# Kernel optimization log

Measured on AMD Instinct MI355X. Metric: run time of the kernel, lower is better.

Reference implementation:

```python
import jax, jax.numpy as jnp
import numpy as np

N_PATCHES = 14
HIDDEN_D = 768
N_HEADS = 12
D_HEAD = HIDDEN_D // N_HEADS
SEQ = N_PATCHES ** 2 + 1  # 197
INPUT_D = 3 * 16 * 16  # c * patch_h * patch_w = 768
LN_EPS = 1e-5


def positional_embeddings(seq_len, d):
    # result[i, j] = sin(i / 10000**(j/d)) if j even else cos(i / 10000**((j-1)/d))
    i = jnp.arange(seq_len, dtype=jnp.float32)[:, None]
    j = jnp.arange(d, dtype=jnp.float32)[None, :]
    even = (jnp.arange(d) % 2 == 0)[None, :]
    denom_even = jnp.power(10000.0, j / d)
    denom_odd = jnp.power(10000.0, (j - 1.0) / d)
    return jnp.where(even, jnp.sin(i / denom_even), jnp.cos(i / denom_odd))


def setup_inputs() -> dict:
    key = jax.random.key(0)
    ks = jax.random.split(key, 12)
    s = 0.02
    return {
        "images": jax.random.normal(ks[0], (128, 3, 224, 224), dtype=jnp.float32),
        "W_map": jax.random.normal(ks[1], (HIDDEN_D, INPUT_D), dtype=jnp.float32) * s,
        "b_map": jax.random.normal(ks[2], (HIDDEN_D,), dtype=jnp.float32) * s,
        "class_token": jax.random.uniform(ks[3], (1, HIDDEN_D), dtype=jnp.float32),
        "ln_w": jnp.ones((SEQ, HIDDEN_D), dtype=jnp.float32),
        "ln_b": jnp.zeros((SEQ, HIDDEN_D), dtype=jnp.float32),
        "Wq": jax.random.normal(ks[4], (N_HEADS, D_HEAD, D_HEAD), dtype=jnp.float32) * s,
        "bq": jax.random.normal(ks[5], (N_HEADS, D_HEAD), dtype=jnp.float32) * s,
        "Wk": jax.random.normal(ks[6], (N_HEADS, D_HEAD, D_HEAD), dtype=jnp.float32) * s,
        "bk": jax.random.normal(ks[7], (N_HEADS, D_HEAD), dtype=jnp.float32) * s,
        "Wv": jax.random.normal(ks[8], (N_HEADS, D_HEAD, D_HEAD), dtype=jnp.float32) * s,
        "bv": jax.random.normal(ks[9], (N_HEADS, D_HEAD), dtype=jnp.float32) * s,
    }


def _forward(images, W_map, b_map, class_token, ln_w, ln_b, Wq, bq, Wk, bk, Wv, bv):
    n = images.shape[0]
    # naive patchify (faithful to source: a plain reshape)
    patches = images.reshape(n, N_PATCHES ** 2, INPUT_D)
    # linear mapper: x @ W.T + b
    tokens = jnp.einsum("npi,di->npd", patches, W_map) + b_map
    # prepend class token
    cls = jnp.broadcast_to(class_token[None], (n, 1, HIDDEN_D))
    tokens = jnp.concatenate([cls, tokens], axis=1)  # [n, SEQ, D]
    # positional embeddings
    tokens = tokens + positional_embeddings(SEQ, HIDDEN_D)[None]
    # LayerNorm over last two dims (SEQ, D) jointly
    mean = jnp.mean(tokens, axis=(-2, -1), keepdims=True)
    var = jnp.var(tokens, axis=(-2, -1), keepdims=True)
    x = (tokens - mean) / jnp.sqrt(var + LN_EPS) * ln_w + ln_b
    # multi-head self-attention (batched over samples and heads)
    xh = x.reshape(n, SEQ, N_HEADS, D_HEAD)  # head-sliced channels
    q = jnp.einsum("bshd,hed->bshe", xh, Wq) + bq[None, None]
    k = jnp.einsum("bshd,hed->bshe", xh, Wk) + bk[None, None]
    v = jnp.einsum("bshd,hed->bshe", xh, Wv) + bv[None, None]
    att = jax.nn.softmax(
        jnp.einsum("bshd,bthd->bhst", q, k) / jnp.sqrt(jnp.float32(D_HEAD)), axis=-1
    )
    msa = jnp.einsum("bhst,bthd->bshd", att, v).reshape(n, SEQ, HIDDEN_D)
    return tokens + msa


def reference(images, W_map, b_map, class_token, ln_w, ln_b, Wq, bq, Wk, bk, Wv, bv):
    return _forward(images, W_map, b_map, class_token, ln_w, ln_b, Wq, bq, Wk, bk, Wv, bv)
```

## Files before the change

kernel.cpp:

```cpp
#include <hip/hip_runtime.h>

typedef float fx4 __attribute__((ext_vector_type(4)));
typedef __bf16 bf16x8 __attribute__((ext_vector_type(8)));
typedef unsigned short ushort8 __attribute__((ext_vector_type(8)));
typedef unsigned int uint2v __attribute__((ext_vector_type(2)));
typedef unsigned int uint4v __attribute__((ext_vector_type(4)));

#define MFMA16(a, b, c) __builtin_amdgcn_mfma_f32_16x16x32_bf16((a), (b), (c), 0, 0, 0)

#if __has_builtin(__builtin_amdgcn_exp2f)
#define EXP2(x) __builtin_amdgcn_exp2f(x)
#else
#define EXP2(x) exp2f(x)
#endif

__device__ __forceinline__ unsigned short f2bf(float f) {
  return __builtin_bit_cast(unsigned short, (__bf16)f);
}

__device__ __forceinline__ ushort8 pack8(fx4 a, fx4 b) {
  ushort8 v;
  v[0] = f2bf(a[0]); v[1] = f2bf(a[1]); v[2] = f2bf(a[2]); v[3] = f2bf(a[3]);
  v[4] = f2bf(b[0]); v[5] = f2bf(b[1]); v[6] = f2bf(b[2]); v[7] = f2bf(b[3]);
  return v;
}

__device__ __forceinline__ uint2v pack2(fx4 v) {
  uint2v r;
  r[0] = (unsigned int)f2bf(v[0]) | ((unsigned int)f2bf(v[1]) << 16);
  r[1] = (unsigned int)f2bf(v[2]) | ((unsigned int)f2bf(v[3]) << 16);
  return r;
}

__device__ __forceinline__ bf16x8 xfrm(uint2v A, uint2v B, int quad, int src0, int src1) {
  uint4v pf;
#pragma unroll
  for (int d = 0; d < 2; d++) {
    int a0 = __shfl((int)A[d], src0, 64);
    int b0 = __shfl((int)B[d], src0, 64);
    pf[d] = (unsigned int)((quad < 2) ? a0 : b0);
    int a1 = __shfl((int)A[d], src1, 64);
    int b1 = __shfl((int)B[d], src1, 64);
    pf[2 + d] = (unsigned int)((quad < 2) ? a1 : b1);
  }
  return __builtin_bit_cast(bf16x8, pf);
}

__device__ __forceinline__ void gl2lds16(const unsigned short* g, void* lds_base) {
  __builtin_amdgcn_global_load_lds(
      (const __attribute__((address_space(1))) void*)(unsigned long long)(g),
      (__attribute__((address_space(3))) void*)(unsigned int)(unsigned long long)(lds_base),
      16, 0, 0);
}

__global__ void k_pe(float* __restrict__ pe, float* __restrict__ sums, float* __restrict__ sqs) {
  int idx = blockIdx.x * 256 + threadIdx.x;
  int s = idx / 768;
  int j = idx - s * 768;
  int jj = j & ~1;
  float ang = (float)s * expf((float)jj * (-9.210340371976184f / 768.0f));
  pe[idx] = (j & 1) ? cosf(ang) : sinf(ang);
  if (blockIdx.x == 0 && threadIdx.x < 128) {
    sums[threadIdx.x] = 0.f;
    sqs[threadIdx.x] = 0.f;
  }
}

__global__ void k_cvt(const float* __restrict__ img, const float* __restrict__ W,
                      unsigned short* __restrict__ imgbf, unsigned short* __restrict__ wbf) {
  size_t i = ((size_t)blockIdx.x * 256 + threadIdx.x) * 8;
  const float* src;
  unsigned short* dst;
  if (i < 19267584) { src = img + i; dst = imgbf + i; }
  else { size_t j = i - 19267584; src = W + j; dst = wbf + j; }
  const fx4* p = (const fx4*)src;
  *(ushort8*)dst = pack8(p[0], p[1]);
}

__global__ void k_wcvt(const float* __restrict__ Wq, const float* __restrict__ Wk,
                       const float* __restrict__ Wv, unsigned short* __restrict__ wqkv) {
  int i = (blockIdx.x * 256 + threadIdx.x) * 8;
  const float* src = (i < 49152) ? (Wq + i) : (i < 98304 ? Wk + (i - 49152) : Wv + (i - 98304));
  const fx4* p = (const fx4*)src;
  *(ushort8*)(wqkv + i) = pack8(p[0], p[1]);
}

__global__ __launch_bounds__(256) void k_tokens(
    const unsigned short* __restrict__ imgbf, const unsigned short* __restrict__ wbf,
    const float* __restrict__ bmap, const float* __restrict__ pe,
    float* __restrict__ out, float* __restrict__ sums, float* __restrict__ sqs) {
  __shared__ __align__(16) ushort8 Sf[16 * 64];
  if (blockIdx.x >= 196) return;
  const int tid = threadIdx.x;
  const int m0 = blockIdx.x * 128;
  const int n0 = blockIdx.y * 128;
  const int lane = tid & 63;
  const int w = tid >> 6;
  const int quad = lane >> 4, l16 = lane & 15;
  const int m_off = (w & 1) * 64, n_off = (w >> 1) * 64;

  fx4 acc[4][4];
#pragma unroll
  for (int i = 0; i < 4; i++)
#pragma unroll
    for (int j = 0; j < 4; j++) acc[i][j] = (fx4){0.f, 0.f, 0.f, 0.f};

  const unsigned short* pA = imgbf + (size_t)(m0 + w * 16 + l16) * 768 + quad * 8;
  const unsigned short* pB = wbf + (size_t)(n0 + w * 16 + l16) * 768 + quad * 8;
  void* lA0 = (void*)&Sf[(w) * 64];
  void* lA1 = (void*)&Sf[(4 + w) * 64];
  void* lB0 = (void*)&Sf[(8 + w) * 64];
  void* lB1 = (void*)&Sf[(12 + w) * 64];

  for (int k0 = 0; k0 < 768; k0 += 32) {
    __syncthreads();
    gl2lds16(pA + k0, lA0);
    gl2lds16(pA + 64 * 768 + k0, lA1);
    gl2lds16(pB + k0, lB0);
    gl2lds16(pB + 64 * 768 + k0, lB1);
    __syncthreads();
    bf16x8 a[4], b[4];
#pragma unroll
    for (int mt = 0; mt < 4; mt++)
      a[mt] = __builtin_bit_cast(bf16x8, Sf[((w & 1) * 4 + mt) * 64 + lane]);
#pragma unroll
    for (int nt = 0; nt < 4; nt++)
      b[nt] = __builtin_bit_cast(bf16x8, Sf[(8 + (w >> 1) * 4 + nt) * 64 + lane]);
#pragma unroll
    for (int mt = 0; mt < 4; mt++)
#pragma unroll
      for (int nt = 0; nt < 4; nt++) acc[mt][nt] = MFMA16(a[mt], b[nt], acc[mt][nt]);
  }

  float s0 = 0.f, q0 = 0.f, s1 = 0.f, q1 = 0.f;
  const int b0 = m0 / 196;
#pragma unroll
  for (int mt = 0; mt < 4; mt++) {
#pragma unroll
    for (int nt = 0; nt < 4; nt++) {
      const int col = n0 + n_off + nt * 16 + l16;
      const float bc = bmap[col];
#pragma unroll
      for (int r = 0; r < 4; r++) {
        const int gm = m0 + m_off + mt * 16 + quad * 4 + r;
        const int bb = gm / 196;
        const int ss = gm - bb * 196 + 1;
        float val = acc[mt][nt][r] + bc + pe[ss * 768 + col];
        out[((size_t)bb * 197 + ss) * 768 + col] = val;
        if (bb == b0) { s0 += val; q0 += val * val; }
        else          { s1 += val; q1 += val * val; }
      }
    }
  }
  for (int off = 32; off > 0; off >>= 1) {
    s0 += __shfl_down(s0, off); q0 += __shfl_down(q0, off);
    s1 += __shfl_down(s1, off); q1 += __shfl_down(q1, off);
  }
  if (lane == 0) {
    atomicAdd(&sums[b0], s0);
    atomicAdd(&sqs[b0], q0);
    if (b0 + 1 < 128) { atomicAdd(&sums[b0 + 1], s1); atomicAdd(&sqs[b0 + 1], q1); }
  }
}

__global__ __launch_bounds__(256) void k_cls(
    const float* __restrict__ ct, const float* __restrict__ pe,
    float* __restrict__ out, float* __restrict__ sums, float* __restrict__ sqs) {
  const int b = blockIdx.x, tid = threadIdx.x;
  float s = 0.f, q = 0.f;
#pragma unroll
  for (int it = 0; it < 3; it++) {
    int j = tid + it * 256;
    float v = ct[j] + pe[j];
    out[(size_t)b * 197 * 768 + j] = v;
    s += v; q += v * v;
  }
  for (int off = 32; off > 0; off >>= 1) { s += __shfl_down(s, off); q += __shfl_down(q, off); }
  __shared__ float rs[4], rq[4];
  int w = tid >> 6;
  if ((tid & 63) == 0) { rs[w] = s; rq[w] = q; }
  __syncthreads();
  if (tid == 0) {
    atomicAdd(&sums[b], rs[0] + rs[1] + rs[2] + rs[3]);
    atomicAdd(&sqs[b], rq[0] + rq[1] + rq[2] + rq[3]);
  }
}

__global__ void k_fin(const float* __restrict__ sums, const float* __restrict__ sqs,
                      float* __restrict__ mr) {
  int i = threadIdx.x;
  const float inv = 1.0f / 151296.0f;
  float m = sums[i] * inv;
  float v = sqs[i] * inv - m * m;
  mr[2 * i] = m;
  mr[2 * i + 1] = rsqrtf(v + 1e-5f);
}

__global__ __launch_bounds__(256, 3) void k_fused(
    const float* tok, const float* __restrict__ mr,
    const float* __restrict__ lnw, const float* __restrict__ lnb,
    const unsigned short* __restrict__ wqkv,
    const float* __restrict__ bq, const float* __restrict__ bk, const float* __restrict__ bv,
    float* out) {
  __shared__ __align__(16) ushort8 Kf[26 * 64];
  __shared__ __align__(16) ushort8 Vf[24 * 64];
  __shared__ __align__(16) ushort8 Vt[4 * 32];
  const int tid = threadIdx.x;
  const int bh = blockIdx.x;
  const int b = bh / 12;
  const int h = bh - b * 12;
  const int lane = tid & 63;
  const int w = tid >> 6;
  const int quad = lane >> 4;
  const int l16 = lane & 15;
  const int src0 = l16 + ((quad & 1) << 5);
  const int src1 = src0 + 16;
  const float mean = mr[2 * b], rstd = mr[2 * b + 1];
  const int hcol = h * 64;

  bf16x8 qfr[4][2];

  bf16x8 wq[4][2], wk[4][2], wv[4][2];
#pragma unroll
  for (int et = 0; et < 4; et++) {
    const int ro = (et * 16 + l16) * 64 + quad * 8;
#pragma unroll
    for (int kk = 0; kk < 2; kk++) {
      wq[et][kk] = *(const bf16x8*)(wqkv + hcol * 64 + ro + kk * 32);
      wk[et][kk] = *(const bf16x8*)(wqkv + 49152 + hcol * 64 + ro + kk * 32);
      wv[et][kk] = *(const bf16x8*)(wqkv + 98304 + hcol * 64 + ro + kk * 32);
    }
  }

#pragma unroll
  for (int pi = 0; pi < 2; pi++) {
    const int jp = w + 4 * pi;
    if (jp <= 6) {
      bf16x8 xf[2][2];
#pragma unroll
      for (int s2 = 0; s2 < 2; s2++) {
        const int tt = 2 * jp + s2;
        if (tt < 13) {
          int ss = tt * 16 + l16;
          ss = (ss < 197) ? ss : 196;
#pragma unroll
          for (int kk = 0; kk < 2; kk++) {
            const int col = hcol + kk * 32 + quad * 8;
            const fx4* px = (const fx4*)(tok + (size_t)(b * 197 + ss) * 768 + col);
            const fx4* pw = (const fx4*)(lnw + (size_t)ss * 768 + col);
            const fx4* pb = (const fx4*)(lnb + (size_t)ss * 768 + col);
            fx4 y0 = (px[0] - mean) * rstd * pw[0] + pb[0];
            fx4 y1 = (px[1] - mean) * rstd * pw[1] + pb[1];
            xf[s2][kk] = __builtin_bit_cast(bf16x8, pack8(y0, y1));
          }
          fx4 aq[4], ak[4];
#pragma unroll
          for (int et = 0; et < 4; et++) {
            aq[et] = (fx4){0.f, 0.f, 0.f, 0.f};
            ak[et] = (fx4){0.f, 0.f, 0.f, 0.f};
          }
#pragma unroll
          for (int kk = 0; kk < 2; kk++)
#pragma unroll
            for (int et = 0; et < 4; et++) {
              aq[et] = MFMA16(wq[et][kk], xf[s2][kk], aq[et]);
              ak[et] = MFMA16(wk[et][kk], xf[s2][kk], ak[et]);
            }
          uint2v qp[4], kp[4];
#pragma unroll
          for (int et = 0; et < 4; et++) {
            fx4 bqv = *(const fx4*)(bq + hcol + et * 16 + quad * 4);
            fx4 bkv = *(const fx4*)(bk + hcol + et * 16 + quad * 4);
            qp[et] = pack2((aq[et] + bqv) * 0.18033688f);
            kp[et] = pack2(ak[et] + bkv);
          }
          const int qi = pi * 2 + s2;
#pragma unroll
          for (int kk = 0; kk < 2; kk++) {
            qfr[qi][kk] = xfrm(qp[2 * kk], qp[2 * kk + 1], quad, src0, src1);
            bf16x8 kfrag = xfrm(kp[2 * kk], kp[2 * kk + 1], quad, src0, src1);
            Kf[(tt * 2 + kk) * 64 + lane] = __builtin_bit_cast(ushort8, kfrag);
          }
        }
      }
      fx4 av[2][4];
#pragma unroll
      for (int s2 = 0; s2 < 2; s2++)
#pragma unroll
        for (int et = 0; et < 4; et++) av[s2][et] = (fx4){0.f, 0.f, 0.f, 0.f};
#pragma unroll
      for (int s2 = 0; s2 < 2; s2++) {
        const int tt = 2 * jp + s2;
        if (tt < 13) {
#pragma unroll
          for (int kk = 0; kk < 2; kk++)
#pragma unroll
            for (int et = 0; et < 4; et++)
              av[s2][et] = MFMA16(xf[s2][kk], wv[et][kk], av[s2][et]);
        }
      }
#pragma unroll
      for (int et = 0; et < 4; et++) {
        const float bvv = bv[hcol + et * 16 + l16];
        fx4 bb4 = (fx4){bvv, bvv, bvv, bvv};
        uint2v v0 = pack2(av[0][et] + bb4);
        uint2v v1 = pack2(av[1][et] + bb4);
        bf16x8 vfrag = xfrm(v0, v1, quad, src0, src1);
        if (jp < 6) Vf[(et * 6 + jp) * 64 + lane] = __builtin_bit_cast(ushort8, vfrag);
        else if (quad < 2) Vt[et * 32 + lane] = __builtin_bit_cast(ushort8, vfrag);
      }
    }
  }
  __syncthreads();

#pragma unroll
  for (int qi = 0; qi < 4; qi++) {
    const int mt = 2 * w + (qi >> 1) * 8 + (qi & 1);
    if (mt < 13) {
      fx4 sacc[13];
#pragma unroll
      for (int nt = 0; nt < 13; nt++) sacc[nt] = (fx4){0.f, 0.f, 0.f, 0.f};
#pragma unroll
      for (int kk = 0; kk < 2; kk++) {
        bf16x8 qf = qfr[qi][kk];
#pragma unroll
        for (int nt = 0; nt < 13; nt++) {
          bf16x8 kf = __builtin_bit_cast(bf16x8, Kf[(nt * 2 + kk) * 64 + lane]);
          sacc[nt] = MFMA16(kf, qf, sacc[nt]);
        }
      }
      float sm = 0.f;
      uint2v pk[13];
#pragma unroll
      for (int nt = 0; nt < 13; nt++) {
        fx4 p;
#pragma unroll
        for (int r = 0; r < 4; r++) {
          const bool valid = (nt < 12) | (quad * 4 + r < 5);
          p[r] = valid ? EXP2(sacc[nt][r]) : 0.f;
          sm += p[r];
        }
        pk[nt] = pack2(p);
      }
      sm += __shfl_xor(sm, 16);
      sm += __shfl_xor(sm, 32);
      const float inv = 1.0f / sm;

      fx4 oacc[4];
#pragma unroll
      for (int et = 0; et < 4; et++) oacc[et] = (fx4){0.f, 0.f, 0.f, 0.f};
#pragma unroll
      for (int kk = 0; kk < 7; kk++) {
        uint4v pf;
        if (kk < 6) {
          const int nA = 2 * kk, nB = 2 * kk + 1;
#pragma unroll
          for (int d = 0; d < 2; d++) {
            int a0 = __shfl((int)pk[nA][d], src0, 64);
            int b0 = __shfl((int)pk[nB][d], src0, 64);
            pf[d] = (unsigned int)((quad < 2) ? a0 : b0);
            int a1 = __shfl((int)pk[nA][d], src1, 64);
            int b1 = __shfl((int)pk[nB][d], src1, 64);
            pf[2 + d] = (unsigned int)((quad < 2) ? a1 : b1);
          }
        } else {
#pragma unroll
          for (int d = 0; d < 2; d++) {
            int a0 = __shfl((int)pk[12][d], src0, 64);
            pf[d] = (quad < 2) ? (unsigned int)a0 : 0u;
            int a1 = __shfl((int)pk[12][d], src1, 64);
            pf[2 + d] = (quad < 2) ? (unsigned int)a1 : 0u;
          }
        }
        bf16x8 pfrag = __builtin_bit_cast(bf16x8, pf);
#pragma unroll
        for (int et = 0; et < 4; et++) {
          bf16x8 vf;
          if (kk < 6) {
            vf = __builtin_bit_cast(bf16x8, Vf[(et * 6 + kk) * 64 + lane]);
          } else if (quad < 2) {
            vf = __builtin_bit_cast(bf16x8, Vt[et * 32 + lane]);
          } else {
            ushort8 z = {0, 0, 0, 0, 0, 0, 0, 0};
            vf = __builtin_bit_cast(bf16x8, z);
          }
          oacc[et] = MFMA16(vf, pfrag, oacc[et]);
        }
      }
      const int sg = mt * 16 + l16;
      if (sg < 197) {
        float* op = out + ((size_t)b * 197 + sg) * 768 + hcol + quad * 4;
#pragma unroll
        for (int et = 0; et < 4; et++) {
          fx4 cur = *(const fx4*)(op + et * 16);
          cur += oacc[et] * inv;
          *(fx4*)(op + et * 16) = cur;
        }
      }
    }
  }
}

extern "C" void kernel_launch(void* const* d_in, const int* in_sizes, int n_in,
                              void* d_out, int out_size, void* d_ws, size_t ws_size,
                              hipStream_t stream) {
  (void)in_sizes; (void)n_in; (void)out_size; (void)ws_size;
  const float* img  = (const float*)d_in[0];
  const float* Wmap = (const float*)d_in[1];
  const float* bmap = (const float*)d_in[2];
  const float* ct   = (const float*)d_in[3];
  const float* lnw  = (const float*)d_in[4];
  const float* lnb  = (const float*)d_in[5];
  const float* Wq   = (const float*)d_in[6];
  const float* bq   = (const float*)d_in[7];
  const float* Wk   = (const float*)d_in[8];
  const float* bk   = (const float*)d_in[9];
  const float* Wv   = (const float*)d_in[10];
  const float* bv   = (const float*)d_in[11];
  float* out = (float*)d_out;

  float* pe   = (float*)d_ws;
  float* sums = pe + 151296;
  float* sqs  = sums + 128;
  float* mr   = sqs + 128;
  unsigned short* wbf   = (unsigned short*)(mr + 256);
  unsigned short* imgbf = wbf + 589824;
  unsigned short* wqkv  = imgbf + (size_t)19267584;

  k_pe<<<591, 256, 0, stream>>>(pe, sums, sqs);
  k_cvt<<<9696, 256, 0, stream>>>(img, Wmap, imgbf, wbf);
  k_wcvt<<<72, 256, 0, stream>>>(Wq, Wk, Wv, wqkv);
  k_tokens<<<dim3(200, 6), 256, 0, stream>>>(imgbf, wbf, bmap, pe, out, sums, sqs);
  k_cls<<<128, 256, 0, stream>>>(ct, pe, out, sums, sqs);
  k_fin<<<1, 128, 0, stream>>>(sums, sqs, mr);
  k_fused<<<1536, 256, 0, stream>>>(out, mr, lnw, lnb, wqkv, bq, bk, bv, out);
}
```

Measured before the change: 358.3 us.

## Use 8-wave blocks in fused attention and permlane32 swaps for fragment transposes

Doubles k_fused's block size to 512 threads so each wave handles one Q/K/V projection tile and at most two query tiles, instead of looping twice with 4 waves. Replaces the four-shuffle-plus-select fragment transpose with one preswap shuffle followed by v_permlane32_swap, which cuts the ds_bpermute count. The residual output tile is now loaded before the attention math so its latency overlaps compute. The larger block and the (512,4) launch bounds put more pressure on registers and change occupancy. The permlane32_swap instruction also requires gfx950 support.

Result: slower. 371.8 us (+3.8%).

```diff
diff --git a/kernel.cpp b/kernel.cpp
--- a/kernel.cpp
+++ b/kernel.cpp
@@ -32,17 +32,19 @@
   return r;
 }
 
-__device__ __forceinline__ bf16x8 xfrm(uint2v A, uint2v B, int quad, int src0, int src1) {
+__device__ __forceinline__ uint2v preswap(uint2v x, int presrc) {
+  uint2v r;
+  r[0] = (unsigned int)__shfl((int)x[0], presrc, 64);
+  r[1] = (unsigned int)__shfl((int)x[1], presrc, 64);
+  return r;
+}
+
+__device__ __forceinline__ bf16x8 xfrm2(uint2v As, uint2v Bs) {
+  unsigned int a0 = As[0], b0 = Bs[0], a1 = As[1], b1 = Bs[1];
+  asm("v_permlane32_swap_b32 %0, %1" : "+v"(a0), "+v"(b0));
+  asm("v_permlane32_swap_b32 %0, %1" : "+v"(a1), "+v"(b1));
   uint4v pf;
-#pragma unroll
-  for (int d = 0; d < 2; d++) {
-    int a0 = __shfl((int)A[d], src0, 64);
-    int b0 = __shfl((int)B[d], src0, 64);
-    pf[d] = (unsigned int)((quad < 2) ? a0 : b0);
-    int a1 = __shfl((int)A[d], src1, 64);
-    int b1 = __shfl((int)B[d], src1, 64);
-    pf[2 + d] = (unsigned int)((quad < 2) ? a1 : b1);
-  }
+  pf[0] = a0; pf[1] = a1; pf[2] = b0; pf[3] = b1;
   return __builtin_bit_cast(bf16x8, pf);
 }
 
@@ -196,7 +198,7 @@
   mr[2 * i + 1] = rsqrtf(v + 1e-5f);
 }
 
-__global__ __launch_bounds__(256, 3) void k_fused(
+__global__ __launch_bounds__(512, 4) void k_fused(
     const float* tok, const float* __restrict__ mr,
     const float* __restrict__ lnw, const float* __restrict__ lnb,
     const unsigned short* __restrict__ wqkv,
@@ -213,110 +215,111 @@
   const int w = tid >> 6;
   const int quad = lane >> 4;
   const int l16 = lane & 15;
-  const int src0 = l16 + ((quad & 1) << 5);
-  const int src1 = src0 + 16;
+  const int presrc = ((quad + 1) & 2) ? (lane ^ 48) : lane;
   const float mean = mr[2 * b], rstd = mr[2 * b + 1];
   const int hcol = h * 64;
 
-  bf16x8 qfr[4][2];
-
-  bf16x8 wq[4][2], wk[4][2], wv[4][2];
-#pragma unroll
-  for (int et = 0; et < 4; et++) {
-    const int ro = (et * 16 + l16) * 64 + quad * 8;
-#pragma unroll
-    for (int kk = 0; kk < 2; kk++) {
-      wq[et][kk] = *(const bf16x8*)(wqkv + hcol * 64 + ro + kk * 32);
-      wk[et][kk] = *(const bf16x8*)(wqkv + 49152 + hcol * 64 + ro + kk * 32);
-      wv[et][kk] = *(const bf16x8*)(wqkv + 98304 + hcol * 64 + ro + kk * 32);
-    }
-  }
-
-#pragma unroll
-  for (int pi = 0; pi < 2; pi++) {
-    const int jp = w + 4 * pi;
-    if (jp <= 6) {
-      bf16x8 xf[2][2];
-#pragma unroll
-      for (int s2 = 0; s2 < 2; s2++) {
-        const int tt = 2 * jp + s2;
-        if (tt < 13) {
-          int ss = tt * 16 + l16;
-          ss = (ss < 197) ? ss : 196;
-#pragma unroll
-          for (int kk = 0; kk < 2; kk++) {
-            const int col = hcol + kk * 32 + quad * 8;
-            const fx4* px = (const fx4*)(tok + (size_t)(b * 197 + ss) * 768 + col);
-            const fx4* pw = (const fx4*)(lnw + (size_t)ss * 768 + col);
-            const fx4* pb = (const fx4*)(lnb + (size_t)ss * 768 + col);
-            fx4 y0 = (px[0] - mean) * rstd * pw[0] + pb[0];
-            fx4 y1 = (px[1] - mean) * rstd * pw[1] + pb[1];
-            xf[s2][kk] = __builtin_bit_cast(bf16x8, pack8(y0, y1));
+  bf16x8 qfr[2][2];
+
+  if (w < 7) {
+    const int jp = w;
+    bf16x8 wq[4][2], wk[4][2], wv[4][2];
+#pragma unroll
+    for (int et = 0; et < 4; et++) {
+      const int ro = (et * 16 + l16) * 64 + quad * 8;
+#pragma unroll
+      for (int kk = 0; kk < 2; kk++) {
+        wq[et][kk] = *(const bf16x8*)(wqkv + hcol * 64 + ro + kk * 32);
+        wk[et][kk] = *(const bf16x8*)(wqkv + 49152 + hcol * 64 + ro + kk * 32);
+        wv[et][kk] = *(const bf16x8*)(wqkv + 98304 + hcol * 64 + ro + kk * 32);
+      }
+    }
+    bf16x8 xf[2][2];
+#pragma unroll
+    for (int s2 = 0; s2 < 2; s2++) {
+      const int tt = 2 * jp + s2;
+      if (tt < 13) {
+        int ss = tt * 16 + l16;
+        ss = (ss < 197) ? ss : 196;
+#pragma unroll
+        for (int kk = 0; kk < 2; kk++) {
+          const int col = hcol + kk * 32 + quad * 8;
+          const fx4* px = (const fx4*)(tok + (size_t)(b * 197 + ss) * 768 + col);
+          const fx4* pw = (const fx4*)(lnw + (size_t)ss * 768 + col);
+          const fx4* pb = (const fx4*)(lnb + (size_t)ss * 768 + col);
+          fx4 y0 = (px[0] - mean) * rstd * pw[0] + pb[0];
+          fx4 y1 = (px[1] - mean) * rstd * pw[1] + pb[1];
+          xf[s2][kk] = __builtin_bit_cast(bf16x8, pack8(y0, y1));
+        }
+        fx4 aq[4], ak[4];
+#pragma unroll
+        for (int et = 0; et < 4; et++) {
+          aq[et] = (fx4){0.f, 0.f, 0.f, 0.f};
+          ak[et] = (fx4){0.f, 0.f, 0.f, 0.f};
+        }
+#pragma unroll
+        for (int kk = 0; kk < 2; kk++)
+#pragma unroll
+          for (int et = 0; et < 4; et++) {
+            aq[et] = MFMA16(wq[et][kk], xf[s2][kk], aq[et]);
+            ak[et] = MFMA16(wk[et][kk], xf[s2][kk], ak[et]);
           }
-          fx4 aq[4], ak[4];
-#pragma unroll
-          for (int et = 0; et < 4; et++) {
-            aq[et] = (fx4){0.f, 0.f, 0.f, 0.f};
-            ak[et] = (fx4){0.f, 0.f, 0.f, 0.f};
-          }
-#pragma unroll
-          for (int kk = 0; kk < 2; kk++)
-#pragma unroll
-            for (int et = 0; et < 4; et++) {
-              aq[et] = MFMA16(wq[et][kk], xf[s2][kk], aq[et]);
-              ak[et] = MFMA16(wk[et][kk], xf[s2][kk], ak[et]);
-            }
-          uint2v qp[4], kp[4];
-#pragma unroll
-          for (int et = 0; et < 4; et++) {
-            fx4 bqv = *(const fx4*)(bq + hcol + et * 16 + quad * 4);
-            fx4 bkv = *(const fx4*)(bk + hcol + et * 16 + quad * 4);
-            qp[et] = pack2((aq[et] + bqv) * 0.18033688f);
-            kp[et] = pack2(ak[et] + bkv);
-          }
-          const int qi = pi * 2 + s2;
-#pragma unroll
-          for (int kk = 0; kk < 2; kk++) {
-            qfr[qi][kk] = xfrm(qp[2 * kk], qp[2 * kk + 1], quad, src0, src1);
-            bf16x8 kfrag = xfrm(kp[2 * kk], kp[2 * kk + 1], quad, src0, src1);
-            Kf[(tt * 2 + kk) * 64 + lane] = __builtin_bit_cast(ushort8, kfrag);
-          }
-        }
-      }
-      fx4 av[2][4];
-#pragma unroll
-      for (int s2 = 0; s2 < 2; s2++)
-#pragma unroll
-        for (int et = 0; et < 4; et++) av[s2][et] = (fx4){0.f, 0.f, 0.f, 0.f};
-#pragma unroll
-      for (int s2 = 0; s2 < 2; s2++) {
-        const int tt = 2 * jp + s2;
-        if (tt < 13) {
-#pragma unroll
-          for (int kk = 0; kk < 2; kk++)
-#pragma unroll
-            for (int et = 0; et < 4; et++)
-              av[s2][et] = MFMA16(xf[s2][kk], wv[et][kk], av[s2][et]);
-        }
-      }
-#pragma unroll
-      for (int et = 0; et < 4; et++) {
-        const float bvv = bv[hcol + et * 16 + l16];
-        fx4 bb4 = (fx4){bvv, bvv, bvv, bvv};
-        uint2v v0 = pack2(av[0][et] + bb4);
-        uint2v v1 = pack2(av[1][et] + bb4);
-        bf16x8 vfrag = xfrm(v0, v1, quad, src0, src1);
-        if (jp < 6) Vf[(et * 6 + jp) * 64 + lane] = __builtin_bit_cast(ushort8, vfrag);
-        else if (quad < 2) Vt[et * 32 + lane] = __builtin_bit_cast(ushort8, vfrag);
-      }
+        uint2v qp[4], kp[4];
+#pragma unroll
+        for (int et = 0; et < 4; et++) {
+          fx4 bqv = *(const fx4*)(bq + hcol + et * 16 + quad * 4);
+          fx4 bkv = *(const fx4*)(bk + hcol + et * 16 + quad * 4);
+          qp[et] = preswap(pack2((aq[et] + bqv) * 0.18033688f), presrc);
+          kp[et] = preswap(pack2(ak[et] + bkv), presrc);
+        }
+#pragma unroll
+        for (int kk = 0; kk < 2; kk++) {
+          qfr[s2][kk] = xfrm2(qp[2 * kk], qp[2 * kk + 1]);
+          bf16x8 kfrag = xfrm2(kp[2 * kk], kp[2 * kk + 1]);
+          Kf[(tt * 2 + kk) * 64 + lane] = __builtin_bit_cast(ushort8, kfrag);
+        }
+      }
+    }
+    fx4 av[2][4];
+#pragma unroll
+    for (int s2 = 0; s2 < 2; s2++)
+#pragma unroll
+      for (int et = 0; et < 4; et++) av[s2][et] = (fx4){0.f, 0.f, 0.f, 0.f};
+#pragma unroll
+    for (int s2 = 0; s2 < 2; s2++) {
+      const int tt = 2 * jp + s2;
+      if (tt < 13) {
+#pragma unroll
+        for (int kk = 0; kk < 2; kk++)
+#pragma unroll
+          for (int et = 0; et < 4; et++)
+            av[s2][et] = MFMA16(xf[s2][kk], wv[et][kk], av[s2][et]);
+      }
+    }
+#pragma unroll
+    for (int et = 0; et < 4; et++) {
+      const float bvv = bv[hcol + et * 16 + l16];
+      fx4 bb4 = (fx4){bvv, bvv, bvv, bvv};
+      uint2v v0 = preswap(pack2(av[0][et] + bb4), presrc);
+      uint2v v1 = preswap(pack2(av[1][et] + bb4), presrc);
+      bf16x8 vfrag = xfrm2(v0, v1);
+      if (jp < 6) Vf[(et * 6 + jp) * 64 + lane] = __builtin_bit_cast(ushort8, vfrag);
+      else if (quad < 2) Vt[et * 32 + lane] = __builtin_bit_cast(ushort8, vfrag);
     }
   }
   __syncthreads();
 
 #pragma unroll
-  for (int qi = 0; qi < 4; qi++) {
-    const int mt = 2 * w + (qi >> 1) * 8 + (qi & 1);
+  for (int qi = 0; qi < 2; qi++) {
+    const int mt = 2 * w + qi;
     if (mt < 13) {
+      const int sg = mt * 16 + l16;
+      const int sgc = (sg < 197) ? sg : 196;
+      float* op = out + ((size_t)b * 197 + sgc) * 768 + hcol + quad * 4;
+      fx4 ocur[4];
+#pragma unroll
+      for (int et = 0; et < 4; et++) ocur[et] = *(const fx4*)(op + et * 16);
+
       fx4 sacc[13];
 #pragma unroll
       for (int nt = 0; nt < 13; nt++) sacc[nt] = (fx4){0.f, 0.f, 0.f, 0.f};
@@ -340,7 +343,7 @@
           p[r] = valid ? EXP2(sacc[nt][r]) : 0.f;
           sm += p[r];
         }
-        pk[nt] = pack2(p);
+        pk[nt] = preswap(pack2(p), presrc);
       }
       sm += __shfl_xor(sm, 16);
       sm += __shfl_xor(sm, 32);
@@ -351,28 +354,13 @@
       for (int et = 0; et < 4; et++) oacc[et] = (fx4){0.f, 0.f, 0.f, 0.f};
 #pragma unroll
       for (int kk = 0; kk < 7; kk++) {
-        uint4v pf;
+        bf16x8 pfrag;
         if (kk < 6) {
-          const int nA = 2 * kk, nB = 2 * kk + 1;
-#pragma unroll
-          for (int d = 0; d < 2; d++) {
-            int a0 = __shfl((int)pk[nA][d], src0, 64);
-            int b0 = __shfl((int)pk[nB][d], src0, 64);
-            pf[d] = (unsigned int)((quad < 2) ? a0 : b0);
-            int a1 = __shfl((int)pk[nA][d], src1, 64);
-            int b1 = __shfl((int)pk[nB][d], src1, 64);
-            pf[2 + d] = (unsigned int)((quad < 2) ? a1 : b1);
-          }
+          pfrag = xfrm2(pk[2 * kk], pk[2 * kk + 1]);
         } else {
-#pragma unroll
-          for (int d = 0; d < 2; d++) {
-            int a0 = __shfl((int)pk[12][d], src0, 64);
-            pf[d] = (quad < 2) ? (unsigned int)a0 : 0u;
-            int a1 = __shfl((int)pk[12][d], src1, 64);
-            pf[2 + d] = (quad < 2) ? (unsigned int)a1 : 0u;
-          }
-        }
-        bf16x8 pfrag = __builtin_bit_cast(bf16x8, pf);
+          uint2v z2; z2[0] = 0u; z2[1] = 0u;
+          pfrag = xfrm2(pk[12], z2);
+        }
 #pragma unroll
         for (int et = 0; et < 4; et++) {
           bf16x8 vf;
@@ -387,14 +375,10 @@
           oacc[et] = MFMA16(vf, pfrag, oacc[et]);
         }
       }
-      const int sg = mt * 16 + l16;
       if (sg < 197) {
-        float* op = out + ((size_t)b * 197 + sg) * 768 + hcol + quad * 4;
 #pragma unroll
         for (int et = 0; et < 4; et++) {
-          fx4 cur = *(const fx4*)(op + et * 16);
-          cur += oacc[et] * inv;
-          *(fx4*)(op + et * 16) = cur;
+          *(fx4*)(op + et * 16) = ocur[et] + oacc[et] * inv;
         }
       }
     }
@@ -433,5 +417,5 @@
   k_tokens<<<dim3(200, 6), 256, 0, stream>>>(imgbf, wbf, bmap, pe, out, sums, sqs);
   k_cls<<<128, 256, 0, stream>>>(ct, pe, out, sums, sqs);
   k_fin<<<1, 128, 0, stream>>>(sums, sqs, mr);
-  k_fused<<<1536, 256, 0, stream>>>(out, mr, lnw, lnb, wqkv, bq, bk, bv, out);
-}
+  k_fused<<<1536, 512, 0, stream>>>(out, mr, lnw, lnb, wqkv, bq, bk, bv, out);
+}
```
